# Kernel optimization log

Measured on AMD Instinct MI355X. Metric: run time of the kernel, lower is better.

Reference implementation:

```python
import jax, jax.numpy as jnp
import numpy as np

N_QUBITS = 8

def _ry(theta):
    # PennyLane RY = exp(-i theta Y/2) = [[c,-s],[s,c]]
    c = jnp.cos(theta / 2).astype(jnp.complex64)
    s = jnp.sin(theta / 2).astype(jnp.complex64)
    return jnp.stack([jnp.stack([c, -s], -1), jnp.stack([s, c], -1)], -2)

def _rz(theta):
    # PennyLane RZ = diag(e^{-i theta/2}, e^{i theta/2})
    ph = jnp.exp(-0.5j * theta.astype(jnp.complex64))
    z = jnp.zeros_like(ph)
    return jnp.stack([jnp.stack([ph, z], -1), jnp.stack([z, jnp.conj(ph)], -1)], -2)

def _apply_1q(state, U, wire):
    # state: (B, 2,...,2); U: (2,2) or (B,2,2)
    state = jnp.moveaxis(state, wire + 1, -1)
    if U.ndim == 3:
        state = jnp.einsum('bij,b...j->b...i', U, state)
    else:
        state = jnp.einsum('ij,b...j->b...i', U, state)
    return jnp.moveaxis(state, -1, wire + 1)

def _apply_cnot(state, c, t):
    state = jnp.moveaxis(state, (c + 1, t + 1), (-2, -1))
    state = jnp.concatenate([state[..., 0:1, :], state[..., 1:2, ::-1]], axis=-2)
    return jnp.moveaxis(state, (-2, -1), (c + 1, t + 1))

def _circuit(angles, qw):
    # angles: (B, 2*n_qubits), qw: (3, n_qubits, 3)
    B = angles.shape[0]
    state = jnp.zeros((B,) + (2,) * N_QUBITS, jnp.complex64)
    state = state.at[(slice(None),) + (0,) * N_QUBITS].set(1.0)
    for i in range(N_QUBITS):
        state = _apply_1q(state, _ry(angles[:, i]), i)
        state = _apply_1q(state, _rz(angles[:, i + N_QUBITS]), i)
    for layer in range(3):
        for i in range(N_QUBITS):
            phi, theta, omega = qw[layer, i]
            U = _rz(omega) @ _ry(theta) @ _rz(phi)  # Rot(phi,theta,omega)
            state = _apply_1q(state, U, i)
        for i in range(N_QUBITS - 1):
            state = _apply_cnot(state, i, i + 1)
        state = _apply_cnot(state, N_QUBITS - 1, 0)
    probs = jnp.abs(state) ** 2  # (B, 2,...,2) real
    expz = []
    for i in range(N_QUBITS):
        p = probs.sum(axis=tuple(a for a in range(1, N_QUBITS + 1) if a != i + 1))
        expz.append(p[:, 0] - p[:, 1])  # <Z_i> = p(0) - p(1)
    return jnp.stack(expz, -1)


def setup_inputs() -> dict:
    key = jax.random.key(0)
    ks = jax.random.split(key, 10)
    B = 16384
    return {
        'x': jax.random.normal(ks[0], (B, 80), jnp.float32),
        'W1': jax.random.normal(ks[1], (64, 80), jnp.float32) * 0.1,
        'b1': jax.random.normal(ks[2], (64,), jnp.float32) * 0.1,
        'W2': jax.random.normal(ks[3], (32, 64), jnp.float32) * 0.1,
        'b2': jax.random.normal(ks[4], (32,), jnp.float32) * 0.1,
        'W3': jax.random.normal(ks[5], (16, 32), jnp.float32) * 0.1,
        'b3': jax.random.normal(ks[6], (16,), jnp.float32) * 0.1,
        'qw': jax.random.normal(ks[7], (3, 8, 3), jnp.float32),
        'Wp': jax.random.normal(ks[8], (128, 8), jnp.float32) * 0.1,
        'bp': jax.random.normal(ks[9], (128,), jnp.float32) * 0.1,
    }


def reference(x, W1, b1, W2, b2, W3, b3, qw, Wp, bp):
    h = jnp.tanh(x @ W1.T + b1)
    h = jnp.tanh(h @ W2.T + b2)
    angles = h @ W3.T + b3          # (B, 16)
    z = _circuit(angles, qw)        # (B, 8) PauliZ expectations
    return z @ Wp.T + bp            # (B, 128)
```

## Files before the change

kernel.cpp:

```cpp
#include <hip/hip_runtime.h>

typedef float v2f __attribute__((ext_vector_type(2)));

#define WPB 4
#define NE  4

__device__ __forceinline__ float xorf(float v, int sb) {
  return __int_as_float(__float_as_int(v) ^ sb);
}
__device__ __forceinline__ v2f xor2(v2f v, int sb) {
  return (v2f){xorf(v.x, sb), xorf(v.y, sb)};
}

__device__ __forceinline__ void pkfma_ip(v2f a, v2f b, v2f& acc) {
  asm("v_pk_fma_f32 %0, %1, %2, %0" : "+v"(acc) : "v"(a), "v"(b));
}
__device__ __forceinline__ v2f pkmul_bl(v2f c, v2f v) {
  v2f r; asm("v_pk_mul_f32 %0, %1, %2 op_sel:[0,0] op_sel_hi:[0,1]"
             : "=v"(r) : "v"(c), "v"(v)); return r;
}
__device__ __forceinline__ void pkfma_bl(v2f c, v2f v, v2f& acc) {
  asm("v_pk_fma_f32 %0, %1, %2, %0 op_sel:[0,0,0] op_sel_hi:[0,1,1]"
      : "+v"(acc) : "v"(c), "v"(v));
}
__device__ __forceinline__ void pkfma_bl_n(v2f c, v2f v, v2f& acc) {
  asm("v_pk_fma_f32 %0, %1, %2, %0 op_sel:[0,0,0] op_sel_hi:[0,1,1] neg_lo:[1,0,0] neg_hi:[1,0,0]"
      : "+v"(acc) : "v"(c), "v"(v));
}
__device__ __forceinline__ void pkfma_bh_i(v2f c, v2f v, v2f& acc) {
  asm("v_pk_fma_f32 %0, %1, %2, %0 op_sel:[1,1,0] op_sel_hi:[1,0,1] neg_lo:[1,0,0]"
      : "+v"(acc) : "v"(c), "v"(v));
}
__device__ __forceinline__ void pkfma_bh_mi(v2f c, v2f v, v2f& acc) {
  asm("v_pk_fma_f32 %0, %1, %2, %0 op_sel:[1,1,0] op_sel_hi:[1,0,1] neg_hi:[1,0,0]"
      : "+v"(acc) : "v"(c), "v"(v));
}
__device__ __forceinline__ v2f cmul(v2f a, v2f b) {
  v2f r = pkmul_bl(a, b);
  pkfma_bh_i(a, b, r);
  return r;
}

template<int M>
__device__ __forceinline__ float xch(float v, int a32) {
  if constexpr (M == 32)
    return __int_as_float(__builtin_amdgcn_ds_bpermute(a32, __float_as_int(v)));
  else if constexpr (M == 16 || M == 4)
    return __int_as_float(__builtin_amdgcn_ds_swizzle(__float_as_int(v), (M << 10) | 0x1f));
  else if constexpr (M == 8) {
    int i = __float_as_int(v);
    return __int_as_float(__builtin_amdgcn_update_dpp(i, i, 0x128, 0xF, 0xF, false));
  } else if constexpr (M == 2) {
    int i = __float_as_int(v);
    return __int_as_float(__builtin_amdgcn_update_dpp(i, i, 0x4E, 0xF, 0xF, false));
  } else {
    int i = __float_as_int(v);
    return __int_as_float(__builtin_amdgcn_update_dpp(i, i, 0xB1, 0xF, 0xF, false));
  }
}
template<int M>
__device__ __forceinline__ v2f xch2(v2f v, int a32) {
  v2f r; r.x = xch<M>(v.x, a32); r.y = xch<M>(v.y, a32); return r;
}
__device__ __forceinline__ v2f bperm2(int addr, v2f v) {
  v2f r;
  r.x = __int_as_float(__builtin_amdgcn_ds_bpermute(addr, __float_as_int(v.x)));
  r.y = __int_as_float(__builtin_amdgcn_ds_bpermute(addr, __float_as_int(v.y)));
  return r;
}

__device__ __forceinline__ void gpair(v2f& a, v2f& b, v2f P1, v2f P2) {
  v2f na = pkmul_bl(P1, a);
  pkfma_bh_i(P1, a, na);
  pkfma_bl(P2, b, na);
  pkfma_bh_i(P2, b, na);
  v2f nb = pkmul_bl(P1, b);
  pkfma_bh_mi(P1, b, nb);
  pkfma_bl_n(P2, a, nb);
  pkfma_bh_i(P2, a, nb);
  a = na; b = nb;
}
__device__ __forceinline__ v2f glane(v2f a, v2f p, v2f P1, v2f P2) {
  v2f t = pkmul_bl(P1, a);
  pkfma_bh_i(P1, a, t);
  pkfma_bl(P2, p, t);
  pkfma_bh_i(P2, p, t);
  return t;
}

__device__ __forceinline__ void build_state(v2f& S0, v2f& S1, v2f& S2, v2f& S3,
                                            const float4* csW, int lane) {
  v2f g2, g3, g4, g5, g6, g7;
  #define BG(q, dst) { float4 c = csW[q]; \
    v2f P1 = (v2f){c.x, c.y}; v2f nc2 = (v2f){-c.z, c.w}; \
    dst = (((lane >> (7 - (q))) & 1) != 0) ? nc2 : P1; }
  BG(2, g2) BG(3, g3) BG(4, g4) BG(5, g5) BG(6, g6) BG(7, g7)
  #undef BG
  v2f common = cmul(cmul(cmul(g2, g3), cmul(g4, g5)), cmul(g6, g7));
  float4 c0 = csW[0], c1 = csW[1];
  v2f P10 = (v2f){c0.x, c0.y}, m0 = (v2f){-c0.z, c0.w};
  v2f P11 = (v2f){c1.x, c1.y}, m1 = (v2f){-c1.z, c1.w};
  S0 = cmul(cmul(P10, P11), common);
  S1 = cmul(cmul(P10, m1 ), common);
  S2 = cmul(cmul(m0 , P11), common);
  S3 = cmul(cmul(m0 , m1 ), common);
}

__device__ __forceinline__ float fast_tanh(float x) {
  float e = __expf(2.f * x);
  return 1.f - 2.f * __builtin_amdgcn_rcpf(e + 1.f);
}
__device__ __forceinline__ v2f vlo(float4 v) { return (v2f){v.x, v.y}; }
__device__ __forceinline__ v2f vhi(float4 v) { return (v2f){v.z, v.w}; }

__global__ void prep_rot_kernel(const float* __restrict__ qw, float* __restrict__ U) {
  int t = threadIdx.x;
  if (t < 24) {
    float phi = qw[t*3+0], theta = qw[t*3+1], omega = qw[t*3+2];
    float st, ct; sincosf(0.5f*theta, &st, &ct);
    float sa, ca; sincosf(0.5f*(phi+omega), &sa, &ca);
    float sd, cd; sincosf(0.5f*(phi-omega), &sd, &cd);
    float4 o; o.x = ct*ca; o.y = -ct*sa; o.z = -st*cd; o.w = -st*sd;
    ((float4*)U)[t] = o;
  }
}

__global__ __launch_bounds__(64*WPB, 4) void qblock_kernel(
    const float* __restrict__ x,  const float* __restrict__ W1, const float* __restrict__ b1,
    const float* __restrict__ W2, const float* __restrict__ b2,
    const float* __restrict__ W3, const float* __restrict__ b3,
    const float* __restrict__ Urot, const float* __restrict__ Wp, const float* __restrict__ bp,
    float* __restrict__ out, int B4)
{
  __shared__ float  h1s[WPB][NE][64];
  __shared__ float  h2s[WPB][NE][32];
  __shared__ v2f    cs [WPB][NE][16];
  __shared__ float4 csW[WPB][NE][8];

  const int lane = threadIdx.x & 63;
  const int wv   = threadIdx.x >> 6;
  int bw = blockIdx.x * WPB + wv;
  if (bw >= B4) bw = B4 - 1;
  bw = __builtin_amdgcn_readfirstlane(bw);
  const int e0 = NE * bw;
  const v2f* Ug2 = (const v2f*)Urot;

  {
    const float4* wr = (const float4*)(W1 + lane * 80);
    float bv = b1[lane];
    v2f a0A = (v2f){bv,0.f}, a1A = (v2f){0.f,0.f};
    v2f a0B = a0A, a1B = a1A, a0C = a0A, a1C = a1A, a0D = a0A, a1D = a1A;
    #pragma unroll
    for (int k = 0; k < 20; ++k) {
      float4 wk = wr[k];
      #define L1E(E, e) { \
        float4 xk = ((const float4*)(x + (size_t)(e0 + (e)) * 80))[k]; \
        pkfma_ip(vlo(xk), vlo(wk), a0##E); pkfma_ip(vhi(xk), vhi(wk), a1##E); }
      L1E(A,0) L1E(B,1) L1E(C,2) L1E(D,3)
      #undef L1E
    }
    h1s[wv][0][lane] = fast_tanh((a0A.x + a0A.y) + (a1A.x + a1A.y));
    h1s[wv][1][lane] = fast_tanh((a0B.x + a0B.y) + (a1B.x + a1B.y));
    h1s[wv][2][lane] = fast_tanh((a0C.x + a0C.y) + (a1C.x + a1C.y));
    h1s[wv][3][lane] = fast_tanh((a0D.x + a0D.y) + (a1D.x + a1D.y));
  }
  __threadfence_block();

  {
    const int ep = lane >> 5, row = lane & 31;
    const float4* wr = (const float4*)(W2 + row * 64);
    const float4* hvA = (const float4*)(&h1s[wv][2*ep+0][0]);
    const float4* hvB = (const float4*)(&h1s[wv][2*ep+1][0]);
    v2f aA0 = (v2f){b2[row], 0.f}, aA1 = (v2f){0.f, 0.f};
    v2f aB0 = aA0, aB1 = aA1;
    #pragma unroll
    for (int k = 0; k < 16; ++k) {
      float4 wk = wr[k], hA = hvA[k], hB = hvB[k];
      pkfma_ip(vlo(hA), vlo(wk), aA0); pkfma_ip(vhi(hA), vhi(wk), aA1);
      pkfma_ip(vlo(hB), vlo(wk), aB0); pkfma_ip(vhi(hB), vhi(wk), aB1);
    }
    h2s[wv][2*ep+0][row] = fast_tanh((aA0.x + aA0.y) + (aA1.x + aA1.y));
    h2s[wv][2*ep+1][row] = fast_tanh((aB0.x + aB0.y) + (aB1.x + aB1.y));
  }
  __threadfence_block();

  {
    const int e = lane >> 4, row = lane & 15;
    const float4* hv = (const float4*)(&h2s[wv][e][0]);
    const float4* wr = (const float4*)(W3 + row * 32);
    v2f ac0 = (v2f){b3[row], 0.f}, ac1 = (v2f){0.f, 0.f};
    #pragma unroll
    for (int k = 0; k < 8; ++k) {
      float4 hk = hv[k], wk = wr[k];
      pkfma_ip(vlo(hk), vlo(wk), ac0);
      pkfma_ip(vhi(hk), vhi(wk), ac1);
    }
    float sh, ch; __sincosf(0.5f * ((ac0.x + ac0.y) + (ac1.x + ac1.y)), &sh, &ch);
    cs[wv][e][row] = (v2f){ch, sh};
  }
  __threadfence_block();

  if (lane < 32) {
    const int e = lane >> 3, k = lane & 7;
    v2f yy = cs[wv][e][k], zz = cs[wv][e][k + 8];
    v2f u1 = (v2f){  yy.x * zz.x, -yy.x * zz.y };
    v2f u2 = (v2f){ -yy.y * zz.x,  yy.y * zz.y };
    v2f cu1 = (v2f){ u1.x, -u1.y };
    v2f cu2 = (v2f){ u2.x, -u2.y };
    v2f r1 = Ug2[2 * k], r2 = Ug2[2 * k + 1];
    v2f P1c = cmul(r1, u1);
    pkfma_bl_n(r2, cu2, P1c);
    pkfma_bh_mi(r2, cu2, P1c);
    v2f P2c = cmul(r1, u2);
    pkfma_bl(r2, cu1, P2c);
    pkfma_bh_i(r2, cu1, P2c);
    csW[wv][e][k] = make_float4(P1c.x, P1c.y, P2c.x, P2c.y);
  }
  __threadfence_block();

  const int a32 = (lane ^ 32) << 2;
  const int sb[6] = { (lane&32)<<26, (lane&16)<<27, (lane&8)<<28,
                      (lane&4)<<29, (lane&2)<<30, (lane&1)<<31 };
  const int addrA = ((lane ^ (lane >> 1)) & 63) << 2;
  const int addrB = addrA ^ 128;

  v2f sA0, sA1, sA2, sA3, sB0, sB1, sB2, sB3;
  v2f sC0, sC1, sC2, sC3, sD0, sD1, sD2, sD3;
  build_state(sA0, sA1, sA2, sA3, &csW[wv][0][0], lane);
  build_state(sB0, sB1, sB2, sB3, &csW[wv][1][0], lane);
  build_state(sC0, sC1, sC2, sC3, &csW[wv][2][0], lane);
  build_state(sD0, sD1, sD2, sD3, &csW[wv][3][0], lane);

  #define RING_ALL { \
    v2f t; \
    t = sA2; sA2 = sA3; sA3 = t;  t = sB2; sB2 = sB3; sB3 = t; \
    t = sC2; sC2 = sC3; sC3 = t;  t = sD2; sD2 = sD3; sD3 = t; \
    v2f qA0 = bperm2(addrA, sA0), qA2 = bperm2(addrA, sA2), \
        qA1 = bperm2(addrB, sA1), qA3 = bperm2(addrB, sA3), \
        qB0 = bperm2(addrA, sB0), qB2 = bperm2(addrA, sB2), \
        qB1 = bperm2(addrB, sB1), qB3 = bperm2(addrB, sB3), \
        qC0 = bperm2(addrA, sC0), qC2 = bperm2(addrA, sC2), \
        qC1 = bperm2(addrB, sC1), qC3 = bperm2(addrB, sC3), \
        qD0 = bperm2(addrA, sD0), qD2 = bperm2(addrA, sD2), \
        qD1 = bperm2(addrB, sD1), qD3 = bperm2(addrB, sD3); \
    bool c0 = (lane & 1) != 0; \
    sA0 = c0 ? qA2 : qA0; sA2 = c0 ? qA0 : qA2; \
    sA1 = c0 ? qA3 : qA1; sA3 = c0 ? qA1 : qA3; \
    sB0 = c0 ? qB2 : qB0; sB2 = c0 ? qB0 : qB2; \
    sB1 = c0 ? qB3 : qB1; sB3 = c0 ? qB1 : qB3; \
    sC0 = c0 ? qC2 : qC0; sC2 = c0 ? qC0 : qC2; \
    sC1 = c0 ? qC3 : qC1; sC3 = c0 ? qC1 : qC3; \
    sD0 = c0 ? qD2 : qD0; sD2 = c0 ? qD0 : qD2; \
    sD1 = c0 ? qD3 : qD1; sD3 = c0 ? qD1 : qD3; }
  RING_ALL

  #define LG01(l, i) { \
    v2f P1 = Ug2[((l)*8+(i))*2], P2 = Ug2[((l)*8+(i))*2+1]; \
    if constexpr ((i) == 0) { \
      gpair(sA0, sA2, P1, P2); gpair(sA1, sA3, P1, P2); \
      gpair(sB0, sB2, P1, P2); gpair(sB1, sB3, P1, P2); \
      gpair(sC0, sC2, P1, P2); gpair(sC1, sC3, P1, P2); \
      gpair(sD0, sD2, P1, P2); gpair(sD1, sD3, P1, P2); \
    } else { \
      gpair(sA0, sA1, P1, P2); gpair(sA2, sA3, P1, P2); \
      gpair(sB0, sB1, P1, P2); gpair(sB2, sB3, P1, P2); \
      gpair(sC0, sC1, P1, P2); gpair(sC2, sC3, P1, P2); \
      gpair(sD0, sD1, P1, P2); gpair(sD2, sD3, P1, P2); } }

  #define LGX(l, i) { \
    v2f P1 = Ug2[((l)*8+(i))*2], P2 = Ug2[((l)*8+(i))*2+1]; \
    P1.y = xorf(P1.y, sb[(i)-2]); P2.x = xorf(P2.x, sb[(i)-2]); \
    v2f pA0 = xch2<(1<<(7-(i)))>(sA0, a32), pA1 = xch2<(1<<(7-(i)))>(sA1, a32), \
        pA2 = xch2<(1<<(7-(i)))>(sA2, a32), pA3 = xch2<(1<<(7-(i)))>(sA3, a32), \
        pB0 = xch2<(1<<(7-(i)))>(sB0, a32), pB1 = xch2<(1<<(7-(i)))>(sB1, a32), \
        pB2 = xch2<(1<<(7-(i)))>(sB2, a32), pB3 = xch2<(1<<(7-(i)))>(sB3, a32), \
        pC0 = xch2<(1<<(7-(i)))>(sC0, a32), pC1 = xch2<(1<<(7-(i)))>(sC1, a32), \
        pC2 = xch2<(1<<(7-(i)))>(sC2, a32), pC3 = xch2<(1<<(7-(i)))>(sC3, a32), \
        pD0 = xch2<(1<<(7-(i)))>(sD0, a32), pD1 = xch2<(1<<(7-(i)))>(sD1, a32), \
        pD2 = xch2<(1<<(7-(i)))>(sD2, a32), pD3 = xch2<(1<<(7-(i)))>(sD3, a32); \
    sA0 = glane(sA0, pA0, P1, P2); sA1 = glane(sA1, pA1, P1, P2); \
    sA2 = glane(sA2, pA2, P1, P2); sA3 = glane(sA3, pA3, P1, P2); \
    sB0 = glane(sB0, pB0, P1, P2); sB1 = glane(sB1, pB1, P1, P2); \
    sB2 = glane(sB2, pB2, P1, P2); sB3 = glane(sB3, pB3, P1, P2); \
    sC0 = glane(sC0, pC0, P1, P2); sC1 = glane(sC1, pC1, P1, P2); \
    sC2 = glane(sC2, pC2, P1, P2); sC3 = glane(sC3, pC3, P1, P2); \
    sD0 = glane(sD0, pD0, P1, P2); sD1 = glane(sD1, pD1, P1, P2); \
    sD2 = glane(sD2, pD2, P1, P2); sD3 = glane(sD3, pD3, P1, P2); }

  LG01(1,0) LG01(1,1) LGX(1,2) LGX(1,3) LGX(1,4) LGX(1,5) LGX(1,6) LGX(1,7)
  RING_ALL
  LG01(2,0) LG01(2,1) LGX(2,2) LGX(2,3) LGX(2,4) LGX(2,5) LGX(2,6) LGX(2,7)
  #undef LG01
  #undef LGX
  #undef RING_ALL

  v2f zu0,zu1,zu2,zu3,zu4,zu5,zu6,zu7;
  v2f zw0,zw1,zw2,zw3,zw4,zw5,zw6,zw7;
  {
    v2f pu0 = (v2f){fmaf(sA0.x,sA0.x,sA0.y*sA0.y), fmaf(sB0.x,sB0.x,sB0.y*sB0.y)};
    v2f pu1 = (v2f){fmaf(sA1.x,sA1.x,sA1.y*sA1.y), fmaf(sB1.x,sB1.x,sB1.y*sB1.y)};
    v2f pu2 = (v2f){fmaf(sA2.x,sA2.x,sA2.y*sA2.y), fmaf(sB2.x,sB2.x,sB2.y*sB2.y)};
    v2f pu3 = (v2f){fmaf(sA3.x,sA3.x,sA3.y*sA3.y), fmaf(sB3.x,sB3.x,sB3.y*sB3.y)};
    v2f pw0 = (v2f){fmaf(sC0.x,sC0.x,sC0.y*sC0.y), fmaf(sD0.x,sD0.x,sD0.y*sD0.y)};
    v2f pw1 = (v2f){fmaf(sC1.x,sC1.x,sC1.y*sC1.y), fmaf(sD1.x,sD1.x,sD1.y*sD1.y)};
    v2f pw2 = (v2f){fmaf(sC2.x,sC2.x,sC2.y*sC2.y), fmaf(sD2.x,sD2.x,sD2.y*sD2.y)};
    v2f pw3 = (v2f){fmaf(sC3.x,sC3.x,sC3.y*sC3.y), fmaf(sD3.x,sD3.x,sD3.y*sD3.y)};
    v2f Eu = (pu0 + pu3) - (pu1 + pu2), Fu = (pu0 + pu2) - (pu1 + pu3);
    v2f Ew = (pw0 + pw3) - (pw1 + pw2), Fw = (pw0 + pw2) - (pw1 + pw3);
    const int pl = (__popc(lane) & 1) << 31;
    v2f Fvu = xor2(Fu, pl), Fvw = xor2(Fw, pl);
    v2f Smu = Eu, Smw = Ew;
    v2f d1u, d2u, d3u, d4u, d5u, d6u, d1w, d2w, d3w, d4w, d5w, d6w;
    { v2f pu = xch2<32>(Smu, a32); v2f pw = xch2<32>(Smw, a32);
      d1u = xor2(Smu - pu, sb[0]); Smu += pu;
      d1w = xor2(Smw - pw, sb[0]); Smw += pw; }
    { v2f pu = xch2<16>(Smu, a32), qu = xch2<16>(d1u, a32);
      v2f pw = xch2<16>(Smw, a32), qw = xch2<16>(d1w, a32);
      Smu += pu; d2u = xor2(d1u - qu, sb[1]); d1u += qu;
      Smw += pw; d2w = xor2(d1w - qw, sb[1]); d1w += qw; }
    { v2f pu = xch2<8>(Smu, a32), qu = xch2<8>(d1u, a32), ru = xch2<8>(d2u, a32);
      v2f pw = xch2<8>(Smw, a32), qw = xch2<8>(d1w, a32), rw = xch2<8>(d2w, a32);
      Smu += pu; d1u += qu; d3u = xor2(d2u - ru, sb[2]); d2u += ru;
      Smw += pw; d1w += qw; d3w = xor2(d2w - rw, sb[2]); d2w += rw; }
    { v2f pu = xch2<4>(Smu, a32), qu = xch2<4>(d1u, a32),
          ru = xch2<4>(d2u, a32), tu = xch2<4>(d3u, a32);
      v2f pw = xch2<4>(Smw, a32), qw = xch2<4>(d1w, a32),
          rw = xch2<4>(d2w, a32), tw = xch2<4>(d3w, a32);
      Smu += pu; d1u += qu; d2u += ru; d4u = xor2(d3u - tu, sb[3]); d3u += tu;
      Smw += pw; d1w += qw; d2w += rw; d4w = xor2(d3w - tw, sb[3]); d3w += tw; }
    { v2f pu = xch2<2>(Smu, a32), qu = xch2<2>(d1u, a32), ru = xch2<2>(d2u, a32),
          tu = xch2<2>(d3u, a32), wu = xch2<2>(d4u, a32);
      v2f pw = xch2<2>(Smw, a32), qw = xch2<2>(d1w, a32), rw = xch2<2>(d2w, a32),
          tw = xch2<2>(d3w, a32), ww = xch2<2>(d4w, a32);
      Smu += pu; d1u += qu; d2u += ru; d3u += tu;
      d5u = xor2(d4u - wu, sb[4]); d4u += wu;
      Smw += pw; d1w += qw; d2w += rw; d3w += tw;
      d5w = xor2(d4w - ww, sb[4]); d4w += ww; }
    { v2f pu = xch2<1>(Smu, a32), qu = xch2<1>(d1u, a32), ru = xch2<1>(d2u, a32),
          tu = xch2<1>(d3u, a32), wu = xch2<1>(d4u, a32), vu = xch2<1>(d5u, a32);
      v2f pw = xch2<1>(Smw, a32), qw = xch2<1>(d1w, a32), rw = xch2<1>(d2w, a32),
          tw = xch2<1>(d3w, a32), ww = xch2<1>(d4w, a32), vw = xch2<1>(d5w, a32);
      Smu += pu; d1u += qu; d2u += ru; d3u += tu; d4u += wu;
      d6u = xor2(d5u - vu, sb[5]); d5u += vu;
      Smw += pw; d1w += qw; d2w += rw; d3w += tw; d4w += ww;
      d6w = xor2(d5w - vw, sb[5]); d5w += vw; }
    Fvu += xch2<32>(Fvu, a32); Fvw += xch2<32>(Fvw, a32);
    Fvu += xch2<16>(Fvu, a32); Fvw += xch2<16>(Fvw, a32);
    Fvu += xch2<8>(Fvu, a32);  Fvw += xch2<8>(Fvw, a32);
    Fvu += xch2<4>(Fvu, a32);  Fvw += xch2<4>(Fvw, a32);
    Fvu += xch2<2>(Fvu, a32);  Fvw += xch2<2>(Fvw, a32);
    Fvu += xch2<1>(Fvu, a32);  Fvw += xch2<1>(Fvw, a32);
    zu0 = Fvu; zu1 = Smu; zu2 = d1u; zu3 = d2u;
    zu4 = d3u; zu5 = d4u; zu6 = d5u; zu7 = d6u;
    zw0 = Fvw; zw1 = Smw; zw2 = d1w; zw3 = d2w;
    zw4 = d3w; zw5 = d4w; zw6 = d5w; zw7 = d6w;
  }

  const int r0 = 2 * lane;
  const float4* wp = (const float4*)(Wp + r0 * 8);
  float4 w0v = wp[0], w1v = wp[1], w2v = wp[2], w3v = wp[3];
  float2 bpv = ((const float2*)bp)[lane];
  #define PROJ_STORE(P, eA, eB) { \
    v2f o0 = (v2f){bpv.x, bpv.x}; \
    v2f o1 = (v2f){bpv.y, bpv.y}; \
    o0 += z##P##0*w0v.x + z##P##1*w0v.y + z##P##2*w0v.z + z##P##3*w0v.w \
        + z##P##4*w1v.x + z##P##5*w1v.y + z##P##6*w1v.z + z##P##7*w1v.w; \
    o1 += z##P##0*w2v.x + z##P##1*w2v.y + z##P##2*w2v.z + z##P##3*w2v.w \
        + z##P##4*w3v.x + z##P##5*w3v.y + z##P##6*w3v.z + z##P##7*w3v.w; \
    ((float2*)(out + (size_t)(e0 + (eA)) * 128))[lane] = make_float2(o0.x, o1.x); \
    ((float2*)(out + (size_t)(e0 + (eB)) * 128))[lane] = make_float2(o0.y, o1.y); }
  PROJ_STORE(u, 0, 1)
  PROJ_STORE(w, 2, 3)
  #undef PROJ_STORE
}

extern "C" void kernel_launch(void* const* d_in, const int* in_sizes, int n_in,
                              void* d_out, int out_size, void* d_ws, size_t ws_size,
                              hipStream_t stream) {
  const float* x  = (const float*)d_in[0];
  const float* W1 = (const float*)d_in[1];
  const float* b1 = (const float*)d_in[2];
  const float* W2 = (const float*)d_in[3];
  const float* b2 = (const float*)d_in[4];
  const float* W3 = (const float*)d_in[5];
  const float* b3 = (const float*)d_in[6];
  const float* qw = (const float*)d_in[7];
  const float* Wp = (const float*)d_in[8];
  const float* bp = (const float*)d_in[9];
  float* out = (float*)d_out;
  float* Urot = (float*)d_ws;

  const int B = in_sizes[0] / 80;
  const int B4 = B / NE;
  prep_rot_kernel<<<1, 64, 0, stream>>>(qw, Urot);
  const int grid = (B4 + WPB - 1) / WPB;
  qblock_kernel<<<grid, 64 * WPB, 0, stream>>>(x, W1, b1, W2, b2, W3, b3,
                                               Urot, Wp, bp, out, B4);
}
```

Before: 41.39 us.

## Stage transposed W1 and W2 in LDS for conflict-free coalesced weight reads

New measurement: 39.99 us (median of 2 runs). -3.4%, faster.

```diff
diff --git a/kernel.cpp b/kernel.cpp
--- a/kernel.cpp
+++ b/kernel.cpp
@@ -132,13 +132,16 @@
     const float* __restrict__ Urot, const float* __restrict__ Wp, const float* __restrict__ bp,
     float* __restrict__ out, int B4)
 {
+  __shared__ v2f    W1t[40 * 64];
+  __shared__ v2f    W2t[32 * 32];
   __shared__ float  h1s[WPB][NE][64];
   __shared__ float  h2s[WPB][NE][32];
   __shared__ v2f    cs [WPB][NE][16];
   __shared__ float4 csW[WPB][NE][8];
 
-  const int lane = threadIdx.x & 63;
-  const int wv   = threadIdx.x >> 6;
+  const int tid  = threadIdx.x;
+  const int lane = tid & 63;
+  const int wv   = tid >> 6;
   int bw = blockIdx.x * WPB + wv;
   if (bw >= B4) bw = B4 - 1;
   bw = __builtin_amdgcn_readfirstlane(bw);
@@ -146,41 +149,59 @@
   const v2f* Ug2 = (const v2f*)Urot;
 
   {
-    const float4* wr = (const float4*)(W1 + lane * 80);
+    const v2f* W1f2 = (const v2f*)W1;
+    #pragma unroll
+    for (int i = 0; i < 10; ++i) {
+      int j = i * 256 + tid;
+      int r = j / 40, kk = j - r * 40;
+      W1t[kk * 64 + r] = W1f2[j];
+    }
+    const v2f* W2f2 = (const v2f*)W2;
+    #pragma unroll
+    for (int i = 0; i < 4; ++i) {
+      int j = i * 256 + tid;
+      int r = j >> 5, kk = j & 31;
+      W2t[kk * 32 + r] = W2f2[j];
+    }
+  }
+  __syncthreads();
+
+  {
+    const v2f* xA = (const v2f*)(x + (size_t)(e0 + 0) * 80);
+    const v2f* xB = (const v2f*)(x + (size_t)(e0 + 1) * 80);
+    const v2f* xC = (const v2f*)(x + (size_t)(e0 + 2) * 80);
+    const v2f* xD = (const v2f*)(x + (size_t)(e0 + 3) * 80);
     float bv = b1[lane];
-    v2f a0A = (v2f){bv,0.f}, a1A = (v2f){0.f,0.f};
-    v2f a0B = a0A, a1B = a1A, a0C = a0A, a1C = a1A, a0D = a0A, a1D = a1A;
-    #pragma unroll
-    for (int k = 0; k < 20; ++k) {
-      float4 wk = wr[k];
-      #define L1E(E, e) { \
-        float4 xk = ((const float4*)(x + (size_t)(e0 + (e)) * 80))[k]; \
-        pkfma_ip(vlo(xk), vlo(wk), a0##E); pkfma_ip(vhi(xk), vhi(wk), a1##E); }
-      L1E(A,0) L1E(B,1) L1E(C,2) L1E(D,3)
-      #undef L1E
+    v2f aA = (v2f){bv, 0.f}, aB = aA, aC = aA, aD = aA;
+    #pragma unroll 8
+    for (int kk = 0; kk < 40; ++kk) {
+      v2f w = W1t[kk * 64 + lane];
+      pkfma_ip(w, xA[kk], aA);
+      pkfma_ip(w, xB[kk], aB);
+      pkfma_ip(w, xC[kk], aC);
+      pkfma_ip(w, xD[kk], aD);
     }
-    h1s[wv][0][lane] = fast_tanh((a0A.x + a0A.y) + (a1A.x + a1A.y));
-    h1s[wv][1][lane] = fast_tanh((a0B.x + a0B.y) + (a1B.x + a1B.y));
-    h1s[wv][2][lane] = fast_tanh((a0C.x + a0C.y) + (a1C.x + a1C.y));
-    h1s[wv][3][lane] = fast_tanh((a0D.x + a0D.y) + (a1D.x + a1D.y));
+    h1s[wv][0][lane] = fast_tanh(aA.x + aA.y);
+    h1s[wv][1][lane] = fast_tanh(aB.x + aB.y);
+    h1s[wv][2][lane] = fast_tanh(aC.x + aC.y);
+    h1s[wv][3][lane] = fast_tanh(aD.x + aD.y);
   }
   __threadfence_block();
 
   {
     const int ep = lane >> 5, row = lane & 31;
-    const float4* wr = (const float4*)(W2 + row * 64);
-    const float4* hvA = (const float4*)(&h1s[wv][2*ep+0][0]);
-    const float4* hvB = (const float4*)(&h1s[wv][2*ep+1][0]);
-    v2f aA0 = (v2f){b2[row], 0.f}, aA1 = (v2f){0.f, 0.f};
-    v2f aB0 = aA0, aB1 = aA1;
-    #pragma unroll
-    for (int k = 0; k < 16; ++k) {
-      float4 wk = wr[k], hA = hvA[k], hB = hvB[k];
-      pkfma_ip(vlo(hA), vlo(wk), aA0); pkfma_ip(vhi(hA), vhi(wk), aA1);
-      pkfma_ip(vlo(hB), vlo(wk), aB0); pkfma_ip(vhi(hB), vhi(wk), aB1);
+    const v2f* hA = (const v2f*)(&h1s[wv][2*ep+0][0]);
+    const v2f* hB = (const v2f*)(&h1s[wv][2*ep+1][0]);
+    float bv = b2[row];
+    v2f aA = (v2f){bv, 0.f}, aB = aA;
+    #pragma unroll 8
+    for (int kk = 0; kk < 32; ++kk) {
+      v2f w = W2t[kk * 32 + row];
+      pkfma_ip(w, hA[kk], aA);
+      pkfma_ip(w, hB[kk], aB);
     }
-    h2s[wv][2*ep+0][row] = fast_tanh((aA0.x + aA0.y) + (aA1.x + aA1.y));
-    h2s[wv][2*ep+1][row] = fast_tanh((aB0.x + aB0.y) + (aB1.x + aB1.y));
+    h2s[wv][2*ep+0][row] = fast_tanh(aA.x + aA.y);
+    h2s[wv][2*ep+1][row] = fast_tanh(aB.x + aB.y);
   }
   __threadfence_block();
 
```
